# Kernel optimization log

Hardware: AMD Instinct MI355X
Metric: run time of the kernel (lower is better)

## Reference

```python
import jax, jax.numpy as jnp
import numpy as np

D_MODEL = 1024
D_STATE = 16
DT_RANK = 64  # d_model // 16 ('auto')
DT_MIN = 0.001
DT_MAX = 0.1


def setup_inputs() -> dict:
    key = jax.random.key(0)
    ks = jax.random.split(key, 7)
    B, S = 2, 2048
    return {
        "x": jax.random.normal(ks[0], (B, S, D_MODEL), jnp.float32),
        "w_in": jax.random.normal(ks[1], (D_MODEL, D_MODEL), jnp.float32) / np.sqrt(D_MODEL).astype(np.float32),
        "w_x": jax.random.normal(ks[2], (D_MODEL, DT_RANK + 2 * D_STATE), jnp.float32) / np.sqrt(D_MODEL).astype(np.float32),
        "w_dt": jax.random.normal(ks[3], (DT_RANK, D_MODEL), jnp.float32) / np.sqrt(DT_RANK).astype(np.float32),
        "b_dt": jnp.zeros((D_MODEL,), jnp.float32),
        "A_log": jax.random.normal(ks[5], (D_MODEL, D_STATE), jnp.float32) * 0.5,
        "Dp": jax.random.normal(ks[6], (D_MODEL,), jnp.float32),
    }


def reference(x, w_in, w_x, w_dt, b_dt, A_log, Dp):
    # x: (b, s, d)
    x_in = jnp.einsum('bsd,de->bse', x, w_in)          # in_proj, (b,s,d_inner=d)
    proj = jnp.einsum('bsd,dp->bsp', x_in, w_x)        # x_proj, (b,s,dt_rank+2n)
    dt_low, Bm, Cm = jnp.split(proj, [DT_RANK, DT_RANK + D_STATE], axis=-1)
    # dt_proj + softplus + range scaling -> (b,s,d)
    dt = jax.nn.softplus(jnp.einsum('bsr,rd->bsd', dt_low, w_dt) + b_dt) * (DT_MAX - DT_MIN) + DT_MIN
    A = -jnp.exp(A_log)                                # (d, n), strictly negative

    b, s, d = x.shape
    h0 = jnp.zeros((b, d, D_STATE), x.dtype)

    # time-major streams for scan
    dt_tm = jnp.swapaxes(dt, 0, 1)     # (s,b,d)
    u_tm = jnp.swapaxes(x_in, 0, 1)    # (s,b,d)
    B_tm = jnp.swapaxes(Bm, 0, 1)      # (s,b,n)
    C_tm = jnp.swapaxes(Cm, 0, 1)      # (s,b,n)

    def step(h, inp):
        dtt, ut, bt, ct = inp
        dA = dtt[:, :, None] * A                      # (b,d,n) = dt[b,d]*A[d,n]
        barA = jnp.exp(dA)
        # bar_B = dA; source sums the input term over channel dim d (keepdim)
        inp_term = jnp.einsum('bdn,bn,bd->bn', dA, bt, ut)  # (b,n)
        h = barA * h + inp_term[:, None, :]           # broadcast over d
        y = jnp.einsum('bdn,bn->bd', h, ct) + Dp * ut # (b,d)
        return h, y

    _, ys = jax.lax.scan(step, h0, (dt_tm, u_tm, B_tm, C_tm))  # ys: (s,b,d)
    return jnp.swapaxes(ys, 0, 1)                     # (b,s,d)
```

## Files before the change

kernel.cpp:

```cpp
#include <hip/hip_runtime.h>
#include <hip/hip_bf16.h>

#define D_MODEL 1024
#define D_STATE 16
#define DT_RANK 64
#define SEQ 2048
#define BATCH 2
#define M_TOTAL 4096
#define CHUNKS 64
#define CLEN 32
#define LOG2E 1.44269504088896f

typedef __bf16 bf16x8 __attribute__((ext_vector_type(8)));
typedef float f32x4 __attribute__((ext_vector_type(4)));

__device__ __forceinline__ unsigned short f2bf(float f) {
    union { float f; unsigned int u; } v; v.f = f;
    unsigned int r = v.u + 0x7FFFu + ((v.u >> 16) & 1u);
    return (unsigned short)(r >> 16);
}
__device__ __forceinline__ float bf2f(unsigned short u) {
    union { unsigned int i; float f; } v; v.i = ((unsigned int)u) << 16; return v.f;
}
__device__ __forceinline__ void gload16(const void* g, void* l) {
    __builtin_amdgcn_global_load_lds(
        (const __attribute__((address_space(1))) unsigned int*)g,
        (__attribute__((address_space(3))) unsigned int*)l, 16, 0, 0);
}
__device__ __forceinline__ float fexp2(float x) { return __builtin_amdgcn_exp2f(x); }

__global__ void __launch_bounds__(256) k_setup(const float* __restrict__ x,
                                               const float* __restrict__ win,
                                               const float* __restrict__ wx,
                                               const float* __restrict__ wdt,
                                               const float* __restrict__ alog,
                                               unsigned short* __restrict__ xb,
                                               unsigned short* __restrict__ bt,
                                               unsigned short* __restrict__ wxT,
                                               unsigned short* __restrict__ wxBC,
                                               unsigned short* __restrict__ wdtT,
                                               float* __restrict__ aneg,
                                               unsigned short* __restrict__ anegT) {
    __shared__ float tile[32][33];
    int blk = blockIdx.x;
    int t = threadIdx.x;
    if (blk < 4096) {
        int i = blk * 256 + t;
        float4 v = reinterpret_cast<const float4*>(x)[i];
        ushort4 o;
        o.x = f2bf(v.x); o.y = f2bf(v.y); o.z = f2bf(v.z); o.w = f2bf(v.w);
        reinterpret_cast<ushort4*>(xb)[i] = o;
    } else if (blk < 5120) {
        int blk2 = blk - 4096;
        int bx = blk2 & 31, by = blk2 >> 5;
        int tx = t & 31, ty = t >> 5;
        int xc = bx * 32 + tx;
#pragma unroll
        for (int j = 0; j < 4; j++)
            tile[ty + 8 * j][tx] = win[(by * 32 + ty + 8 * j) * D_MODEL + xc];
        __syncthreads();
        int x2 = by * 32 + tx;
#pragma unroll
        for (int j = 0; j < 4; j++)
            bt[(bx * 32 + ty + 8 * j) * D_MODEL + x2] = f2bf(tile[tx][ty + 8 * j]);
    } else if (blk < 5376) {
        int idx = (blk - 5120) * 256 + t;
        int e = idx & 1023, p = idx >> 10;
        wxT[p * D_MODEL + e] = f2bf(wx[e * 96 + p]);
    } else if (blk < 5504) {
        int idx = (blk - 5376) * 256 + t;
        int e = idx & 1023, p = idx >> 10;
        wxBC[p * D_MODEL + e] = f2bf(wx[e * 96 + 64 + p]);
    } else if (blk < 5568) {
        int i = (blk - 5504) * 256 + t;
        float v = -expf(alog[i]);
        aneg[i] = v * LOG2E;
        anegT[(i & 15) * D_MODEL + (i >> 4)] = f2bf(v);
    } else {
        int idx = (blk - 5568) * 256 + t;
        int d = idx & 1023, k = idx >> 10;
        wdtT[d * DT_RANK + k] = f2bf(wdt[k * D_MODEL + d]);
    }
}

__global__ void __launch_bounds__(256) k_gemm_xin(const unsigned short* __restrict__ xb,
                                                  const unsigned short* __restrict__ bt,
                                                  unsigned short* __restrict__ xinb) {
    __shared__ unsigned short sA[2][64 * 64];
    __shared__ unsigned short sB[2][128 * 64];
    int bid = blockIdx.x;
    int m0 = (bid & 63) * 64;
    int n0 = (bid >> 6) * 128;
    int t = threadIdx.x;
    int lane = t & 63;
    int w = t >> 6;
    int wm = (w >> 1) * 32, wn = (w & 1) * 64;
    int c = lane & 15, q = lane >> 4;

    const unsigned short* gA[2];
    const unsigned short* gB[4];
#pragma unroll
    for (int L = 0; L < 2; L++) {
        int s = L * 256 + t;
        int row = s >> 3, ch = (s & 7) ^ (row & 7);
        gA[L] = xb + (m0 + row) * D_MODEL + ch * 8;
    }
#pragma unroll
    for (int L = 0; L < 4; L++) {
        int s = L * 256 + t;
        int row = s >> 3, ch = (s & 7) ^ (row & 7);
        gB[L] = bt + (n0 + row) * D_MODEL + ch * 8;
    }

    f32x4 acc[2][4] = {};
    {
        char* la = (char*)&sA[0][0] + w * 1024;
        char* lb = (char*)&sB[0][0] + w * 1024;
#pragma unroll
        for (int L = 0; L < 2; L++) gload16(gA[L], la + L * 4096);
#pragma unroll
        for (int L = 0; L < 4; L++) gload16(gB[L], lb + L * 4096);
    }
    int cur = 0;
    for (int it = 0; it < 16; it++) {
        __syncthreads();
        if (it + 1 < 16) {
            int kn = (it + 1) * 64;
            char* la = (char*)&sA[cur ^ 1][0] + w * 1024;
            char* lb = (char*)&sB[cur ^ 1][0] + w * 1024;
#pragma unroll
            for (int L = 0; L < 2; L++) gload16(gA[L] + kn, la + L * 4096);
#pragma unroll
            for (int L = 0; L < 4; L++) gload16(gB[L] + kn, lb + L * 4096);
        }
#pragma unroll
        for (int kk = 0; kk < 2; kk++) {
            int perm = (((kk << 2) | q) ^ (c & 7)) << 3;
            bf16x8 af[2], bfr[4];
#pragma unroll
            for (int i = 0; i < 2; i++)
                af[i] = *reinterpret_cast<const bf16x8*>(&sA[cur][(wm + i * 16 + c) * 64 + perm]);
#pragma unroll
            for (int j = 0; j < 4; j++)
                bfr[j] = *reinterpret_cast<const bf16x8*>(&sB[cur][(wn + j * 16 + c) * 64 + perm]);
#pragma unroll
            for (int i = 0; i < 2; i++)
#pragma unroll
                for (int j = 0; j < 4; j++)
                    acc[i][j] = __builtin_amdgcn_mfma_f32_16x16x32_bf16(bfr[j], af[i], acc[i][j], 0, 0, 0);
        }
        cur ^= 1;
    }
#pragma unroll
    for (int i = 0; i < 2; i++) {
        int row = m0 + wm + i * 16 + c;
#pragma unroll
        for (int j = 0; j < 4; j++) {
            int col = n0 + wn + j * 16 + q * 4;
            ushort4 o;
            o.x = f2bf(acc[i][j][0]); o.y = f2bf(acc[i][j][1]);
            o.z = f2bf(acc[i][j][2]); o.w = f2bf(acc[i][j][3]);
            *reinterpret_cast<ushort4*>(&xinb[row * D_MODEL + col]) = o;
        }
    }
}

__global__ void __launch_bounds__(256) k_xlow(const unsigned short* __restrict__ xinb,
                                              const unsigned short* __restrict__ wxT,
                                              float* __restrict__ xlp) {
    int bid = blockIdx.x;
    int m0 = (bid & 31) * 128;
    int ks = bid >> 5;
    int kbase = ks * 128;
    int t = threadIdx.x;
    int lane = t & 63, w = t >> 6;
    int c = lane & 15, q = lane >> 4;
    int mw = m0 + w * 32;
    f32x4 acc[2][4] = {};
    const unsigned short* pa0 = xinb + (mw + c) * D_MODEL + kbase + q * 8;
    const unsigned short* pa1 = pa0 + 16 * D_MODEL;
    const unsigned short* pw = wxT + c * D_MODEL + kbase + q * 8;
#pragma unroll
    for (int k0 = 0; k0 < 128; k0 += 32) {
        bf16x8 a0 = *reinterpret_cast<const bf16x8*>(pa0 + k0);
        bf16x8 a1 = *reinterpret_cast<const bf16x8*>(pa1 + k0);
#pragma unroll
        for (int j = 0; j < 4; j++) {
            bf16x8 wf = *reinterpret_cast<const bf16x8*>(pw + j * 16 * D_MODEL + k0);
            acc[0][j] = __builtin_amdgcn_mfma_f32_16x16x32_bf16(wf, a0, acc[0][j], 0, 0, 0);
            acc[1][j] = __builtin_amdgcn_mfma_f32_16x16x32_bf16(wf, a1, acc[1][j], 0, 0, 0);
        }
    }
#pragma unroll
    for (int i = 0; i < 2; i++) {
        int row = mw + i * 16 + c;
#pragma unroll
        for (int j = 0; j < 4; j++)
            *reinterpret_cast<f32x4*>(&xlp[(ks * M_TOTAL + row) * DT_RANK + j * 16 + q * 4]) = acc[i][j];
    }
}

__global__ void __launch_bounds__(256) k_gemm_dt(const float* __restrict__ xlp,
                                                 const unsigned short* __restrict__ wdtT,
                                                 const float* __restrict__ bdt,
                                                 unsigned short* __restrict__ dtb) {
    __shared__ unsigned short sA[128 * 64];
    int bid = blockIdx.x;
    int m0 = (bid & 31) * 128;
    int n0 = (bid >> 5) * 128;
    int t = threadIdx.x;
    int lane = t & 63, w = t >> 6;
    int c = lane & 15, q = lane >> 4;

    {
        int row = t >> 1, half = t & 1;
        int gbase = (m0 + row) * DT_RANK;
#pragma unroll
        for (int ch = 0; ch < 4; ch++) {
            int col8 = half * 4 + ch;
            f32x4 s0 = {}, s1 = {};
#pragma unroll
            for (int ksi = 0; ksi < 8; ksi++) {
                const f32x4* p = reinterpret_cast<const f32x4*>(
                    xlp + ksi * (M_TOTAL * DT_RANK) + gbase + col8 * 8);
                s0 += p[0];
                s1 += p[1];
            }
            int swz = col8 ^ (row & 7);
            ushort4 lo, hi;
            lo.x = f2bf(s0[0]); lo.y = f2bf(s0[1]); lo.z = f2bf(s0[2]); lo.w = f2bf(s0[3]);
            hi.x = f2bf(s1[0]); hi.y = f2bf(s1[1]); hi.z = f2bf(s1[2]); hi.w = f2bf(s1[3]);
            *reinterpret_cast<ushort4*>(&sA[row * 64 + swz * 8]) = lo;
            *reinterpret_cast<ushort4*>(&sA[row * 64 + swz * 8 + 4]) = hi;
        }
    }
    __syncthreads();

    int mw = m0 + w * 32;
    f32x4 acc[2][8] = {};
#pragma unroll
    for (int kk = 0; kk < 2; kk++) {
        bf16x8 af[2];
#pragma unroll
        for (int i = 0; i < 2; i++)
            af[i] = *reinterpret_cast<const bf16x8*>(
                &sA[(w * 32 + i * 16 + c) * 64 + ((((kk << 2) | q)) ^ (c & 7)) * 8]);
#pragma unroll
        for (int j = 0; j < 8; j++) {
            bf16x8 bfr = *reinterpret_cast<const bf16x8*>(
                &wdtT[(n0 + j * 16 + c) * DT_RANK + kk * 32 + q * 8]);
            acc[0][j] = __builtin_amdgcn_mfma_f32_16x16x32_bf16(bfr, af[0], acc[0][j], 0, 0, 0);
            acc[1][j] = __builtin_amdgcn_mfma_f32_16x16x32_bf16(bfr, af[1], acc[1][j], 0, 0, 0);
        }
    }
#pragma unroll
    for (int i = 0; i < 2; i++) {
        int row = mw + i * 16 + c;
#pragma unroll
        for (int j = 0; j < 8; j++) {
            int dcol = n0 + j * 16 + q * 4;
            float4 bv = *reinterpret_cast<const float4*>(&bdt[dcol]);
            ushort4 o;
            {
                float xv = acc[i][j][0] + bv.x;
                float sp = fmaxf(xv, 0.f) + __logf(1.f + __expf(-fabsf(xv)));
                o.x = f2bf(sp * 0.099f + 0.001f);
            }
            {
                float xv = acc[i][j][1] + bv.y;
                float sp = fmaxf(xv, 0.f) + __logf(1.f + __expf(-fabsf(xv)));
                o.y = f2bf(sp * 0.099f + 0.001f);
            }
            {
                float xv = acc[i][j][2] + bv.z;
                float sp = fmaxf(xv, 0.f) + __logf(1.f + __expf(-fabsf(xv)));
                o.z = f2bf(sp * 0.099f + 0.001f);
            }
            {
                float xv = acc[i][j][3] + bv.w;
                float sp = fmaxf(xv, 0.f) + __logf(1.f + __expf(-fabsf(xv)));
                o.w = f2bf(sp * 0.099f + 0.001f);
            }
            *reinterpret_cast<ushort4*>(&dtb[row * D_MODEL + dcol]) = o;
        }
    }
}

__global__ void __launch_bounds__(256) k_bcw(const unsigned short* __restrict__ xinb,
                                             const unsigned short* __restrict__ dtb,
                                             const unsigned short* __restrict__ wxBC,
                                             const unsigned short* __restrict__ anegT,
                                             float* __restrict__ bcp,
                                             float* __restrict__ wpp) {
    int bid = blockIdx.x;
    int m0 = (bid & 31) * 128;
    int ks = bid >> 5;
    int kbase = ks * 128;
    int t = threadIdx.x;
    int lane = t & 63, w = t >> 6;
    int c = lane & 15, q = lane >> 4;
    int mw = m0 + w * 32;
    f32x4 accb[2][2] = {};
    f32x4 accw[2] = {};
    const unsigned short* pa0 = xinb + (mw + c) * D_MODEL + kbase + q * 8;
    const unsigned short* pa1 = pa0 + 16 * D_MODEL;
    const unsigned short* pt0 = dtb + (mw + c) * D_MODEL + kbase + q * 8;
    const unsigned short* pt1 = pt0 + 16 * D_MODEL;
    const unsigned short* pb0 = wxBC + c * D_MODEL + kbase + q * 8;
    const unsigned short* pb1 = pb0 + 16 * D_MODEL;
    const unsigned short* pA = anegT + c * D_MODEL + kbase + q * 8;
#pragma unroll
    for (int k0 = 0; k0 < 128; k0 += 32) {
        bf16x8 a0 = *reinterpret_cast<const bf16x8*>(pa0 + k0);
        bf16x8 a1 = *reinterpret_cast<const bf16x8*>(pa1 + k0);
        bf16x8 t0 = *reinterpret_cast<const bf16x8*>(pt0 + k0);
        bf16x8 t1 = *reinterpret_cast<const bf16x8*>(pt1 + k0);
        bf16x8 b0 = *reinterpret_cast<const bf16x8*>(pb0 + k0);
        bf16x8 b1 = *reinterpret_cast<const bf16x8*>(pb1 + k0);
        bf16x8 bA = *reinterpret_cast<const bf16x8*>(pA + k0);
        bf16x8 g0, g1;
#pragma unroll
        for (int e = 0; e < 8; e++) {
            g0[e] = (__bf16)((float)t0[e] * (float)a0[e]);
            g1[e] = (__bf16)((float)t1[e] * (float)a1[e]);
        }
        accb[0][0] = __builtin_amdgcn_mfma_f32_16x16x32_bf16(b0, a0, accb[0][0], 0, 0, 0);
        accb[0][1] = __builtin_amdgcn_mfma_f32_16x16x32_bf16(b1, a0, accb[0][1], 0, 0, 0);
        accb[1][0] = __builtin_amdgcn_mfma_f32_16x16x32_bf16(b0, a1, accb[1][0], 0, 0, 0);
        accb[1][1] = __builtin_amdgcn_mfma_f32_16x16x32_bf16(b1, a1, accb[1][1], 0, 0, 0);
        accw[0] = __builtin_amdgcn_mfma_f32_16x16x32_bf16(bA, g0, accw[0], 0, 0, 0);
        accw[1] = __builtin_amdgcn_mfma_f32_16x16x32_bf16(bA, g1, accw[1], 0, 0, 0);
    }
#pragma unroll
    for (int i = 0; i < 2; i++) {
        int row = mw + i * 16 + c;
#pragma unroll
        for (int j = 0; j < 2; j++)
            *reinterpret_cast<f32x4*>(&bcp[(ks * M_TOTAL + row) * 32 + j * 16 + q * 4]) = accb[i][j];
        *reinterpret_cast<f32x4*>(&wpp[(ks * M_TOTAL + row) * 16 + q * 4]) = accw[i];
    }
}

__global__ void __launch_bounds__(256) k_scan1(const unsigned short* __restrict__ dtb,
                                               const float* __restrict__ bcp,
                                               const float* __restrict__ wpp,
                                               const float* __restrict__ aneg,
                                               float* __restrict__ h_loc,
                                               float* __restrict__ dtsum) {
    __shared__ unsigned short s_dt[16][256];
    __shared__ float s_w[16][16];
    int dc = blockIdx.x & 3;
    int c = (blockIdx.x >> 2) & (CHUNKS - 1);
    int b = blockIdx.x >> 8;
    int tid = threadIdx.x;
    int d = dc * 256 + tid;
    float Ad[16];
    const float4* ar = reinterpret_cast<const float4*>(aneg + d * 16);
#pragma unroll
    for (int j = 0; j < 4; j++) {
        float4 a4 = ar[j];
        Ad[4 * j + 0] = a4.x; Ad[4 * j + 1] = a4.y;
        Ad[4 * j + 2] = a4.z; Ad[4 * j + 3] = a4.w;
    }
    float h[16];
#pragma unroll
    for (int n = 0; n < 16; n++) h[n] = 0.f;
    float dts = 0.f;

    int r8 = tid >> 5, col8 = (tid & 31) * 8;
    for (int t0 = 0; t0 < CLEN; t0 += 16) {
        __syncthreads();
        int rowbase = b * SEQ + c * CLEN + t0;
        *reinterpret_cast<uint4*>(&s_dt[r8][col8]) =
            *reinterpret_cast<const uint4*>(dtb + (rowbase + r8) * D_MODEL + dc * 256 + col8);
        *reinterpret_cast<uint4*>(&s_dt[8 + r8][col8]) =
            *reinterpret_cast<const uint4*>(dtb + (rowbase + 8 + r8) * D_MODEL + dc * 256 + col8);
        {
            int r = tid >> 4, n = tid & 15;
            int row = rowbase + r;
            float sB = 0.f, sw = 0.f;
#pragma unroll
            for (int ks = 0; ks < 8; ks++) {
                sB += bcp[(ks * M_TOTAL + row) * 32 + n];
                sw += wpp[(ks * M_TOTAL + row) * 16 + n];
            }
            s_w[r][n] = sB * sw;
        }
        __syncthreads();
        for (int r = 0; r < 16; r++) {
            float dtv = bf2f(s_dt[r][tid]);
            dts += dtv;
#pragma unroll
            for (int n = 0; n < 16; n++) {
                float ba = fexp2(dtv * Ad[n]);
                h[n] = fmaf(ba, h[n], s_w[r][n]);
            }
        }
    }
    int base = ((b * CHUNKS + c) * D_MODEL + d) * 16;
#pragma unroll
    for (int j = 0; j < 4; j++) {
        f32x4 v = {h[4 * j], h[4 * j + 1], h[4 * j + 2], h[4 * j + 3]};
        *reinterpret_cast<f32x4*>(h_loc + base + 4 * j) = v;
    }
    dtsum[(b * CHUNKS + c) * D_MODEL + d] = dts;
}

__global__ void __launch_bounds__(128) k_scan2(float* __restrict__ h_inout,
                                               const float* __restrict__ dtsum,
                                               const float* __restrict__ aneg) {
    int idx = blockIdx.x * 128 + threadIdx.x;
    int n = idx & 15;
    int d = (idx >> 4) & (D_MODEL - 1);
    int b = idx >> 14;
    float A = aneg[d * 16 + n];
    float H = 0.f;
    int off0 = b * CHUNKS * D_MODEL + d;
#pragma unroll 1
    for (int g = 0; g < CHUNKS; g += 8) {
        float hl[8], ds[8];
#pragma unroll
        for (int j = 0; j < 8; j++) {
            int off = off0 + (g + j) * D_MODEL;
            hl[j] = h_inout[off * 16 + n];
            ds[j] = dtsum[off];
        }
#pragma unroll
        for (int j = 0; j < 8; j++) {
            int off = off0 + (g + j) * D_MODEL;
            float P = fexp2(ds[j] * A);
            h_inout[off * 16 + n] = H;
            H = fmaf(P, H, hl[j]);
        }
    }
}

__global__ void __launch_bounds__(256) k_scan3(const unsigned short* __restrict__ dtb,
                                               const unsigned short* __restrict__ xinb,
                                               const float* __restrict__ bcp,
                                               const float* __restrict__ wpp,
                                               const float* __restrict__ aneg,
                                               const float* __restrict__ dp,
                                               const float* __restrict__ H_in,
                                               float* __restrict__ out) {
    __shared__ unsigned short s_dt[16][256], s_u[16][256];
    __shared__ float s_w[16][16], s_c[16][16];
    int dc = blockIdx.x & 3;
    int c = (blockIdx.x >> 2) & (CHUNKS - 1);
    int b = blockIdx.x >> 8;
    int tid = threadIdx.x;
    int d = dc * 256 + tid;
    float Ad[16];
    const float4* ar = reinterpret_cast<const float4*>(aneg + d * 16);
#pragma unroll
    for (int j = 0; j < 4; j++) {
        float4 a4 = ar[j];
        Ad[4 * j + 0] = a4.x; Ad[4 * j + 1] = a4.y;
        Ad[4 * j + 2] = a4.z; Ad[4 * j + 3] = a4.w;
    }
    float Dpd = dp[d];
    float h[16];
    int base = ((b * CHUNKS + c) * D_MODEL + d) * 16;
#pragma unroll
    for (int j = 0; j < 4; j++) {
        f32x4 v = *reinterpret_cast<const f32x4*>(H_in + base + 4 * j);
        h[4 * j] = v[0]; h[4 * j + 1] = v[1]; h[4 * j + 2] = v[2]; h[4 * j + 3] = v[3];
    }

    int r8 = tid >> 5, col8 = (tid & 31) * 8;
    for (int t0 = 0; t0 < CLEN; t0 += 16) {
        __syncthreads();
        int rowbase = b * SEQ + c * CLEN + t0;
        *reinterpret_cast<uint4*>(&s_dt[r8][col8]) =
            *reinterpret_cast<const uint4*>(dtb + (rowbase + r8) * D_MODEL + dc * 256 + col8);
        *reinterpret_cast<uint4*>(&s_dt[8 + r8][col8]) =
            *reinterpret_cast<const uint4*>(dtb + (rowbase + 8 + r8) * D_MODEL + dc * 256 + col8);
        *reinterpret_cast<uint4*>(&s_u[r8][col8]) =
            *reinterpret_cast<const uint4*>(xinb + (rowbase + r8) * D_MODEL + dc * 256 + col8);
        *reinterpret_cast<uint4*>(&s_u[8 + r8][col8]) =
            *reinterpret_cast<const uint4*>(xinb + (rowbase + 8 + r8) * D_MODEL + dc * 256 + col8);
        {
            int r = tid >> 4, n = tid & 15;
            int row = rowbase + r;
            float sB = 0.f, sw = 0.f, sC = 0.f;
#pragma unroll
            for (int ks = 0; ks < 8; ks++) {
                sB += bcp[(ks * M_TOTAL + row) * 32 + n];
                sC += bcp[(ks * M_TOTAL + row) * 32 + 16 + n];
                sw += wpp[(ks * M_TOTAL + row) * 16 + n];
            }
            s_w[r][n] = sB * sw;
            s_c[r][n] = sC;
        }
        __syncthreads();
        for (int r = 0; r < 16; r++) {
            float dtv = bf2f(s_dt[r][tid]), uv = bf2f(s_u[r][tid]);
            float y = Dpd * uv;
#pragma unroll
            for (int n = 0; n < 16; n++) {
                float ba = fexp2(dtv * Ad[n]);
                h[n] = fmaf(ba, h[n], s_w[r][n]);
                y = fmaf(h[n], s_c[r][n], y);
            }
            out[(rowbase + r) * D_MODEL + d] = y;
        }
    }
}

extern "C" void kernel_launch(void* const* d_in, const int* in_sizes, int n_in,
                              void* d_out, int out_size, void* d_ws, size_t ws_size,
                              hipStream_t stream) {
    const float* x     = (const float*)d_in[0];
    const float* w_in  = (const float*)d_in[1];
    const float* w_x   = (const float*)d_in[2];
    const float* w_dt  = (const float*)d_in[3];
    const float* b_dt  = (const float*)d_in[4];
    const float* A_log = (const float*)d_in[5];
    const float* Dp    = (const float*)d_in[6];
    float* out = (float*)d_out;

    char* ws = (char*)d_ws;
    unsigned short* xb   = (unsigned short*)(ws + 0);
    unsigned short* bt   = (unsigned short*)(ws + 8388608);
    unsigned short* xinb = (unsigned short*)(ws + 10485760);
    unsigned short* dtb  = (unsigned short*)(ws + 18874368);
    float* xlp           = (float*)(ws + 27262976);
    float* bcp           = (float*)(ws + 27262976);
    float* wpp           = (float*)(ws + 31457280);
    unsigned short* wxT  = (unsigned short*)(ws + 35651584);
    unsigned short* wxBC = (unsigned short*)(ws + 35782656);
    unsigned short* wdtT = (unsigned short*)(ws + 35848192);
    float* aneg          = (float*)(ws + 35979264);
    unsigned short* anegT= (unsigned short*)(ws + 36044800);
    float* h_loc         = (float*)(ws + 0);
    float* dtsum         = (float*)(ws + 8388608);

    k_setup<<<5824, 256, 0, stream>>>(x, w_in, w_x, w_dt, A_log, xb, bt, wxT, wxBC, wdtT, aneg, anegT);
    k_gemm_xin<<<512, 256, 0, stream>>>(xb, bt, xinb);
    k_xlow<<<256, 256, 0, stream>>>(xinb, wxT, xlp);
    k_gemm_dt<<<256, 256, 0, stream>>>(xlp, wdtT, b_dt, dtb);
    k_bcw<<<256, 256, 0, stream>>>(xinb, dtb, wxBC, anegT, bcp, wpp);
    k_scan1<<<BATCH * CHUNKS * 4, 256, 0, stream>>>(dtb, bcp, wpp, aneg, h_loc, dtsum);
    k_scan2<<<256, 128, 0, stream>>>(h_loc, dtsum, aneg);
    k_scan3<<<BATCH * CHUNKS * 4, 256, 0, stream>>>(dtb, xinb, bcp, wpp, aneg, Dp, h_loc, out);
}
```

Baseline: 175.4 us.

## Drop split-K in x_proj low-rank GEMM, write bf16 result directly

The dt_low projection kernel no longer splits K into 8 slices that write fp32 partials. Each block now computes full-K results for 64 rows and stores them as bf16, and the dt GEMM loads that bf16 tile straight into swizzled shared memory with async copies instead of summing 8 partials. This removes the partial-sum write and read traffic and the reduction step. The cost is only 64 blocks on a large GPU, each running a long serial K loop, so latency and occupancy may suffer.

```diff
diff --git a/kernel.cpp b/kernel.cpp
--- a/kernel.cpp
+++ b/kernel.cpp
@@ -167,40 +167,34 @@
 
 __global__ void __launch_bounds__(256) k_xlow(const unsigned short* __restrict__ xinb,
                                               const unsigned short* __restrict__ wxT,
-                                              float* __restrict__ xlp) {
-    int bid = blockIdx.x;
-    int m0 = (bid & 31) * 128;
-    int ks = bid >> 5;
-    int kbase = ks * 128;
+                                              unsigned short* __restrict__ xlow) {
+    int m0 = blockIdx.x * 64;
     int t = threadIdx.x;
     int lane = t & 63, w = t >> 6;
     int c = lane & 15, q = lane >> 4;
-    int mw = m0 + w * 32;
-    f32x4 acc[2][4] = {};
-    const unsigned short* pa0 = xinb + (mw + c) * D_MODEL + kbase + q * 8;
-    const unsigned short* pa1 = pa0 + 16 * D_MODEL;
-    const unsigned short* pw = wxT + c * D_MODEL + kbase + q * 8;
-#pragma unroll
-    for (int k0 = 0; k0 < 128; k0 += 32) {
-        bf16x8 a0 = *reinterpret_cast<const bf16x8*>(pa0 + k0);
-        bf16x8 a1 = *reinterpret_cast<const bf16x8*>(pa1 + k0);
+    int row = m0 + w * 16 + c;
+    f32x4 acc[4] = {};
+    const unsigned short* pa = xinb + row * D_MODEL + q * 8;
+    const unsigned short* pw = wxT + c * D_MODEL + q * 8;
+#pragma unroll 4
+    for (int k0 = 0; k0 < D_MODEL; k0 += 32) {
+        bf16x8 a0 = *reinterpret_cast<const bf16x8*>(pa + k0);
 #pragma unroll
         for (int j = 0; j < 4; j++) {
             bf16x8 wf = *reinterpret_cast<const bf16x8*>(pw + j * 16 * D_MODEL + k0);
-            acc[0][j] = __builtin_amdgcn_mfma_f32_16x16x32_bf16(wf, a0, acc[0][j], 0, 0, 0);
-            acc[1][j] = __builtin_amdgcn_mfma_f32_16x16x32_bf16(wf, a1, acc[1][j], 0, 0, 0);
-        }
-    }
-#pragma unroll
-    for (int i = 0; i < 2; i++) {
-        int row = mw + i * 16 + c;
-#pragma unroll
-        for (int j = 0; j < 4; j++)
-            *reinterpret_cast<f32x4*>(&xlp[(ks * M_TOTAL + row) * DT_RANK + j * 16 + q * 4]) = acc[i][j];
-    }
-}
-
-__global__ void __launch_bounds__(256) k_gemm_dt(const float* __restrict__ xlp,
+            acc[j] = __builtin_amdgcn_mfma_f32_16x16x32_bf16(wf, a0, acc[j], 0, 0, 0);
+        }
+    }
+#pragma unroll
+    for (int j = 0; j < 4; j++) {
+        ushort4 o;
+        o.x = f2bf(acc[j][0]); o.y = f2bf(acc[j][1]);
+        o.z = f2bf(acc[j][2]); o.w = f2bf(acc[j][3]);
+        *reinterpret_cast<ushort4*>(&xlow[row * DT_RANK + j * 16 + q * 4]) = o;
+    }
+}
+
+__global__ void __launch_bounds__(256) k_gemm_dt(const unsigned short* __restrict__ xlow,
                                                  const unsigned short* __restrict__ wdtT,
                                                  const float* __restrict__ bdt,
                                                  unsigned short* __restrict__ dtb) {
@@ -213,25 +207,12 @@
     int c = lane & 15, q = lane >> 4;
 
     {
-        int row = t >> 1, half = t & 1;
-        int gbase = (m0 + row) * DT_RANK;
-#pragma unroll
-        for (int ch = 0; ch < 4; ch++) {
-            int col8 = half * 4 + ch;
-            f32x4 s0 = {}, s1 = {};
-#pragma unroll
-            for (int ksi = 0; ksi < 8; ksi++) {
-                const f32x4* p = reinterpret_cast<const f32x4*>(
-                    xlp + ksi * (M_TOTAL * DT_RANK) + gbase + col8 * 8);
-                s0 += p[0];
-                s1 += p[1];
-            }
-            int swz = col8 ^ (row & 7);
-            ushort4 lo, hi;
-            lo.x = f2bf(s0[0]); lo.y = f2bf(s0[1]); lo.z = f2bf(s0[2]); lo.w = f2bf(s0[3]);
-            hi.x = f2bf(s1[0]); hi.y = f2bf(s1[1]); hi.z = f2bf(s1[2]); hi.w = f2bf(s1[3]);
-            *reinterpret_cast<ushort4*>(&sA[row * 64 + swz * 8]) = lo;
-            *reinterpret_cast<ushort4*>(&sA[row * 64 + swz * 8 + 4]) = hi;
+        char* la = (char*)&sA[0] + w * 1024;
+#pragma unroll
+        for (int L = 0; L < 4; L++) {
+            int s = L * 256 + t;
+            int row = s >> 3, ch = (s & 7) ^ (row & 7);
+            gload16(xlow + (m0 + row) * DT_RANK + ch * 8, la + L * 4096);
         }
     }
     __syncthreads();
@@ -524,9 +505,9 @@
     unsigned short* bt   = (unsigned short*)(ws + 8388608);
     unsigned short* xinb = (unsigned short*)(ws + 10485760);
     unsigned short* dtb  = (unsigned short*)(ws + 18874368);
-    float* xlp           = (float*)(ws + 27262976);
     float* bcp           = (float*)(ws + 27262976);
     float* wpp           = (float*)(ws + 31457280);
+    unsigned short* xlow = (unsigned short*)(ws + 33554432);
     unsigned short* wxT  = (unsigned short*)(ws + 35651584);
     unsigned short* wxBC = (unsigned short*)(ws + 35782656);
     unsigned short* wdtT = (unsigned short*)(ws + 35848192);
@@ -537,8 +518,8 @@
 
     k_setup<<<5824, 256, 0, stream>>>(x, w_in, w_x, w_dt, A_log, xb, bt, wxT, wxBC, wdtT, aneg, anegT);
     k_gemm_xin<<<512, 256, 0, stream>>>(xb, bt, xinb);
-    k_xlow<<<256, 256, 0, stream>>>(xinb, wxT, xlp);
-    k_gemm_dt<<<256, 256, 0, stream>>>(xlp, wdtT, b_dt, dtb);
+    k_xlow<<<64, 256, 0, stream>>>(xinb, wxT, xlow);
+    k_gemm_dt<<<256, 256, 0, stream>>>(xlow, wdtT, b_dt, dtb);
     k_bcw<<<256, 256, 0, stream>>>(xinb, dtb, wxBC, anegT, bcp, wpp);
     k_scan1<<<BATCH * CHUNKS * 4, 256, 0, stream>>>(dtb, bcp, wpp, aneg, h_loc, dtsum);
     k_scan2<<<256, 128, 0, stream>>>(h_loc, dtsum, aneg);
```

New measurement: 175.8 us. Within noise of the previous version (+0.2%).
